# Optimization experiments

Measured on AMD Instinct MI355X. Metric: run time of the kernel, lower is better.

The kernel has to match this reference:

```python
import jax, jax.numpy as jnp
import numpy as np

B, L, H, KV, D, HID = 2, 2048, 16, 4, 128, 2048
EPS = 1e-6
ROPE_BASE = 10000.0


def _rotate_half(x):
    x1, x2 = jnp.split(x, 2, axis=-1)
    return jnp.concatenate((-x2, x1), axis=-1)


def _rms_norm(x, w):
    xf = x.astype(jnp.float32)
    var = jnp.mean(xf * xf, axis=-1, keepdims=True)
    return w * (xf * jax.lax.rsqrt(var + EPS)).astype(x.dtype)


def setup_inputs() -> dict:
    key = jax.random.key(0)
    ks = jax.random.split(key, 6)
    hidden_states = jax.random.normal(ks[0], (B, L, HID), dtype=jnp.float32)
    # rotary embeddings (standard rope table)
    inv_freq = 1.0 / (ROPE_BASE ** (jnp.arange(0, D, 2, dtype=jnp.float32) / D))
    pos = jnp.arange(L, dtype=jnp.float32)
    freqs = pos[:, None] * inv_freq[None, :]          # [L, D/2]
    emb = jnp.concatenate((freqs, freqs), axis=-1)    # [L, D]
    cos = jnp.broadcast_to(jnp.cos(emb)[None], (B, L, D))
    sin = jnp.broadcast_to(jnp.sin(emb)[None], (B, L, D))
    s = 0.02
    Wq = jax.random.normal(ks[1], (HID, H * D), dtype=jnp.float32) * s
    Wk = jax.random.normal(ks[2], (HID, KV * D), dtype=jnp.float32) * s
    Wv = jax.random.normal(ks[3], (HID, KV * D), dtype=jnp.float32) * s
    Wo = jax.random.normal(ks[4], (H * D, HID), dtype=jnp.float32) * s
    q_norm_w = jnp.ones((D,), dtype=jnp.float32)
    k_norm_w = jnp.ones((D,), dtype=jnp.float32)
    return {"hidden_states": hidden_states, "cos": cos, "sin": sin,
            "Wq": Wq, "Wk": Wk, "Wv": Wv, "Wo": Wo,
            "q_norm_w": q_norm_w, "k_norm_w": k_norm_w}


def reference(hidden_states, cos, sin, Wq, Wk, Wv, Wo, q_norm_w, k_norm_w):
    scale = D ** -0.5
    n_rep = H // KV
    q = (hidden_states @ Wq).reshape(B, L, H, D)
    k = (hidden_states @ Wk).reshape(B, L, KV, D)
    v = (hidden_states @ Wv).reshape(B, L, KV, D)
    q = _rms_norm(q, q_norm_w).transpose(0, 2, 1, 3)   # [B,H,L,D]
    k = _rms_norm(k, k_norm_w).transpose(0, 2, 1, 3)   # [B,KV,L,D]
    v = v.transpose(0, 2, 1, 3)                         # [B,KV,L,D]
    c = cos[:, None]                                    # [B,1,L,D]
    s = sin[:, None]
    q = q * c + _rotate_half(q) * s
    k = k * c + _rotate_half(k) * s
    # GQA without materializing repeated K/V: group query heads per kv head.
    qg = q.reshape(B, KV, n_rep, L, D)
    scores = jnp.einsum('bgrld,bgmd->bgrlm', qg, k) * scale
    attn = jax.nn.softmax(scores, axis=-1)
    out = jnp.einsum('bgrlm,bgmd->bgrld', attn, v)      # [B,KV,n_rep,L,D]
    out = out.reshape(B, H, L, D).transpose(0, 2, 1, 3).reshape(B, L, H * D)
    return out @ Wo
```

## Files before the change

kernel.cpp:

```cpp
#include <hip/hip_runtime.h>

typedef unsigned short u16;
typedef unsigned int u32;
typedef short bf16x8 __attribute__((ext_vector_type(8)));
typedef float f32x4 __attribute__((ext_vector_type(4)));

#define B_ 2
#define L_ 2048
#define H_ 16
#define KV_ 4
#define D_ 128
#define HID_ 2048

#define QSCALE (0.08838834764831845f * 1.4426950408889634f)
#define SMAX 17.0f

__device__ __forceinline__ u16 f2bf(float f) {
  union { float f; u32 u; } v; v.f = f;
  u32 u = v.u;
  return (u16)((u + 0x7FFFu + ((u >> 16) & 1u)) >> 16);
}
__device__ __forceinline__ float bf2f(u16 h) {
  union { u32 u; float f; } v; v.u = ((u32)h) << 16;
  return v.f;
}
__device__ __forceinline__ u32 pkbf(float a, float b) {
  union { float f; u32 u; } x, y; x.f = a; y.f = b;
  return ((x.u + 0x8000u) >> 16) | ((y.u + 0x8000u) & 0xffff0000u);
}
__device__ __forceinline__ void gl_lds16(const void* g, void* l) {
  __builtin_amdgcn_global_load_lds((__attribute__((address_space(1))) void*)(g),
                                   (__attribute__((address_space(3))) void*)(l),
                                   16, 0, 0);
}

__global__ void k_f2b(const float* __restrict__ src, u16* __restrict__ dst, int n4) {
  int i = blockIdx.x * 256 + threadIdx.x;
  if (i >= n4) return;
  float4 v = ((const float4*)src)[i];
  u32 a = (u32)f2bf(v.x) | ((u32)f2bf(v.y) << 16);
  u32 b = (u32)f2bf(v.z) | ((u32)f2bf(v.w) << 16);
  ((uint2*)dst)[i] = make_uint2(a, b);
}

__global__ void k_tconv_all(const float* __restrict__ Wq, const float* __restrict__ Wk,
                            const float* __restrict__ Wv, const float* __restrict__ Wo,
                            u16* __restrict__ Wtqkv, u16* __restrict__ Wto) {
  __shared__ float t[32][33];
  int id = blockIdx.x;
  const float* src; u16* dst; int C; int ct, rt;
  if (id < 4096)      { src = Wq; dst = Wtqkv;               C = 2048; ct = id & 63; rt = id >> 6; }
  else if (id < 5120) { id -= 4096; src = Wk; dst = Wtqkv + 2048 * 2048; C = 512; ct = id & 15; rt = id >> 4; }
  else if (id < 6144) { id -= 5120; src = Wv; dst = Wtqkv + 2560 * 2048; C = 512; ct = id & 15; rt = id >> 4; }
  else                { id -= 6144; src = Wo; dst = Wto;     C = 2048; ct = id & 63; rt = id >> 6; }
  const int R = 2048;
  int c0 = ct * 32, r0 = rt * 32;
  for (int i = threadIdx.y; i < 32; i += 8)
    t[i][threadIdx.x] = src[(size_t)(r0 + i) * C + c0 + threadIdx.x];
  __syncthreads();
  for (int i = threadIdx.y; i < 32; i += 8)
    dst[(size_t)(c0 + i) * R + r0 + threadIdx.x] = f2bf(t[threadIdx.x][i]);
}

template <int OUT_BF16>
__global__ __launch_bounds__(256, 3) void k_gemm_bt(
    const u16* __restrict__ A, const u16* __restrict__ Bt, void* __restrict__ Cv,
    int M, int N, int K) {
  __shared__ u16 smem[16384];
  u16* As = smem;
  u16* Bs = smem + 8192;
  const int tid = threadIdx.x;
  const int wave = tid >> 6, lane = tid & 63;
  const int wr = wave >> 1, wc = wave & 1;
  const int quad = lane >> 4, fm = lane & 15;
  const int m0 = blockIdx.y * 128, n0 = blockIdx.x * 128;
  f32x4 acc[4][4];
  for (int i = 0; i < 4; ++i)
    for (int j = 0; j < 4; ++j)
      for (int r = 0; r < 4; ++r) acc[i][j][r] = 0.0f;

  const int lrow = lane >> 3;
  const int lcol = (lane & 7) * 8;
  const int fk = quad * 8;

  for (int kt = 0; kt < K; kt += 64) {
    for (int p = 0; p < 4; ++p) {
      int roff = wave * 32 + p * 8 + lrow;
      gl_lds16(A + (size_t)(m0 + roff) * K + kt + lcol,
               As + wave * 2048 + p * 512 + lane * 8);
      gl_lds16(Bt + (size_t)(n0 + roff) * K + kt + lcol,
               Bs + wave * 2048 + p * 512 + lane * 8);
    }
    __syncthreads();
    for (int s = 0; s < 2; ++s) {
      bf16x8 af[4], bfr[4];
      for (int i = 0; i < 4; ++i)
        af[i] = *(const bf16x8*)(As + (wr * 64 + i * 16 + fm) * 64 + s * 32 + fk);
      for (int j = 0; j < 4; ++j)
        bfr[j] = *(const bf16x8*)(Bs + (wc * 64 + j * 16 + fm) * 64 + s * 32 + fk);
      for (int i = 0; i < 4; ++i)
        for (int j = 0; j < 4; ++j)
          acc[i][j] = __builtin_amdgcn_mfma_f32_16x16x32_bf16(af[i], bfr[j],
                                                              acc[i][j], 0, 0, 0);
    }
    __syncthreads();
  }

  if (OUT_BF16) {
    u16* Cs = smem;
    for (int hh = 0; hh < 2; ++hh) {
      if (hh) __syncthreads();
      if (wr == hh)
        for (int i = 0; i < 4; ++i)
          for (int j = 0; j < 4; ++j)
            for (int r = 0; r < 4; ++r)
              Cs[(i * 16 + quad * 4 + r) * 136 + wc * 64 + j * 16 + fm] =
                  f2bf(acc[i][j][r]);
      __syncthreads();
      for (int it = 0; it < 4; ++it) {
        int row = it * 16 + (tid >> 4);
        int col = (tid & 15) * 8;
        uint4 v = *(const uint4*)(Cs + row * 136 + col);
        *(uint4*)((u16*)Cv + (size_t)(m0 + hh * 64 + row) * N + n0 + col) = v;
      }
    }
  } else {
    float* Cf = (float*)smem;
    for (int p = 0; p < 4; ++p) {
      if (p) __syncthreads();
      if (wr == (p >> 1))
        for (int ii = 0; ii < 2; ++ii) {
          int i = 2 * (p & 1) + ii;
          for (int j = 0; j < 4; ++j)
            for (int r = 0; r < 4; ++r)
              Cf[(ii * 16 + quad * 4 + r) * 132 + wc * 64 + j * 16 + fm] =
                  acc[i][j][r];
        }
      __syncthreads();
      for (int it = 0; it < 4; ++it) {
        int row = it * 8 + (tid >> 5);
        int col = (tid & 31) * 4;
        float4 v = *(const float4*)(Cf + row * 132 + col);
        *(float4*)((float*)Cv + (size_t)(m0 + p * 32 + row) * N + n0 + col) = v;
      }
    }
  }
}

__global__ __launch_bounds__(256) void k_norm_rope(
    const u16* __restrict__ qkv, const float* __restrict__ cosp,
    const float* __restrict__ sinp, const float* __restrict__ qw,
    const float* __restrict__ kw, u16* __restrict__ Qb, u16* __restrict__ Kb,
    u16* __restrict__ Vtb) {
  int wid = blockIdx.x * 4 + (threadIdx.x >> 6);
  int lane = threadIdx.x & 63;
  int tok = wid / 24, unit = wid % 24;
  int b = tok >> 11, l = tok & 2047;
  const u16* row = qkv + (size_t)tok * 3072;
  int d0 = lane * 2;
  if (unit < 20) {
    int isq = unit < 16;
    int col = isq ? unit * 128 : 2048 + (unit - 16) * 128;
    u32 u = *(const u32*)(row + col + d0);
    float x0 = bf2f((u16)(u & 0xffff)), x1 = bf2f((u16)(u >> 16));
    float ss = x0 * x0 + x1 * x1;
    for (int m = 1; m < 64; m <<= 1) ss += __shfl_xor(ss, m);
    float rr = rsqrtf(ss * (1.0f / 128.0f) + 1e-6f);
    const float* wv = isq ? qw : kw;
    float n0 = x0 * rr * wv[d0], n1 = x1 * rr * wv[d0 + 1];
    float p0 = __shfl_xor(n0, 32), p1 = __shfl_xor(n1, 32);
    float sgn = (lane < 32) ? -1.0f : 1.0f;
    const float* cb = cosp + (size_t)tok * 128;
    const float* sb = sinp + (size_t)tok * 128;
    float o0 = n0 * cb[d0] + sgn * p0 * sb[d0];
    float o1 = n1 * cb[d0 + 1] + sgn * p1 * sb[d0 + 1];
    if (isq) {
      o0 *= QSCALE;
      o1 *= QSCALE;
      u32 packed = (u32)f2bf(o0) | ((u32)f2bf(o1) << 16);
      size_t off = (((size_t)(b * H_ + unit)) * L_ + l) * D_ + d0;
      *(u32*)(Qb + off) = packed;
    } else {
      u32 packed = (u32)f2bf(o0) | ((u32)f2bf(o1) << 16);
      size_t off = (((size_t)(b * KV_ + (unit - 16))) * L_ + l) * D_ + d0;
      *(u32*)(Kb + off) = packed;
    }
  } else {
    int g = unit - 20;
    int lp = (l & ~31) | (((l >> 2) & 3) << 3) | (((l >> 4) & 1) << 2) | (l & 3);
    size_t base = (((size_t)(b * KV_ + g)) * D_ + d0) * L_ + lp;
    Vtb[base] = row[2560 + g * 128 + d0];
    Vtb[base + L_] = row[2560 + g * 128 + d0 + 1];
  }
}

__global__ __launch_bounds__(256, 2) void k_attn(const u16* __restrict__ Qb,
                                                 const u16* __restrict__ Kb,
                                                 const u16* __restrict__ Vtb,
                                                 u16* __restrict__ AO) {
  __shared__ u16 smem[16384];
  u16* Ks = smem;
  u16* Vs = smem + 8192;
  const int tid = threadIdx.x, wave = tid >> 6, lane = tid & 63;
  const int quad = lane >> 4, fm = lane & 15;
  const int f7 = fm & 7;
  const int qt = blockIdx.x, bh = blockIdx.y;
  const int b = bh >> 4, h = bh & 15, g = h >> 2;
  const u16* Kg = Kb + ((size_t)(b * KV_ + g)) * L_ * D_;
  const u16* Vg = Vtb + ((size_t)(b * KV_ + g)) * D_ * L_;

  const u16* Qg = Qb + ((size_t)bh * L_ + qt * 128 + wave * 32 + fm) * D_;
  bf16x8 qf1[4], qf2[4];
  for (int ks = 0; ks < 4; ++ks) {
    qf1[ks] = *(const bf16x8*)(Qg + ks * 32 + quad * 8);
    qf2[ks] = *(const bf16x8*)(Qg + 16 * D_ + ks * 32 + quad * 8);
  }

  f32x4 o1[8], o2[8];
  for (int f = 0; f < 8; ++f)
    for (int r = 0; r < 4; ++r) { o1[f][r] = 0.0f; o2[f][r] = 0.0f; }
  float lr1 = 0.0f, lr2 = 0.0f;

  const int eK = wave * 2048 + (lane << 3);
  const int cK = lane & 15;
  const int cV = lane & 7;
  for (int kt = 0; kt < 32; ++kt) {
    __syncthreads();
    for (int p = 0; p < 4; ++p) {
      int e = eK + p * 512;
      int rowK = e >> 7;
      int gK = (cK & 8) | ((cK & 7) ^ (rowK & 7));
      gl_lds16(Kg + (size_t)(kt * 64 + rowK) * 128 + gK * 8, Ks + e);
      int rowV = e >> 6;
      int gV = cV ^ (rowV & 7);
      gl_lds16(Vg + (size_t)rowV * L_ + kt * 64 + gV * 8, Vs + e);
    }
    __syncthreads();

    f32x4 s1[4], s2[4];
    for (int n = 0; n < 4; ++n)
      for (int r = 0; r < 4; ++r) { s1[n][r] = 0.0f; s2[n][r] = 0.0f; }
    for (int ks = 0; ks < 4; ++ks) {
      int c = 4 * ks + quad;
      int cp = (c & 8) | ((c & 7) ^ f7);
      for (int n = 0; n < 4; ++n) {
        bf16x8 kf = *(const bf16x8*)(Ks + (n * 16 + fm) * 128 + cp * 8);
        s1[n] = __builtin_amdgcn_mfma_f32_16x16x32_bf16(kf, qf1[ks], s1[n], 0, 0, 0);
        s2[n] = __builtin_amdgcn_mfma_f32_16x16x32_bf16(kf, qf2[ks], s2[n], 0, 0, 0);
      }
    }

    u32 pk1[4][2], pk2[4][2];
    float rs1 = 0.0f, rs2 = 0.0f;
    for (int n = 0; n < 4; ++n) {
      float a0 = __builtin_amdgcn_exp2f(s1[n][0] - SMAX);
      float a1 = __builtin_amdgcn_exp2f(s1[n][1] - SMAX);
      float a2 = __builtin_amdgcn_exp2f(s1[n][2] - SMAX);
      float a3 = __builtin_amdgcn_exp2f(s1[n][3] - SMAX);
      rs1 += (a0 + a1) + (a2 + a3);
      pk1[n][0] = pkbf(a0, a1);
      pk1[n][1] = pkbf(a2, a3);
      float b0 = __builtin_amdgcn_exp2f(s2[n][0] - SMAX);
      float b1 = __builtin_amdgcn_exp2f(s2[n][1] - SMAX);
      float b2 = __builtin_amdgcn_exp2f(s2[n][2] - SMAX);
      float b3 = __builtin_amdgcn_exp2f(s2[n][3] - SMAX);
      rs2 += (b0 + b1) + (b2 + b3);
      pk2[n][0] = pkbf(b0, b1);
      pk2[n][1] = pkbf(b2, b3);
    }
    lr1 += rs1;
    lr2 += rs2;

    for (int ks2 = 0; ks2 < 2; ++ks2) {
      union { u32 u[4]; bf16x8 v; } pa1, pa2;
      pa1.u[0] = pk1[2 * ks2][0];
      pa1.u[1] = pk1[2 * ks2][1];
      pa1.u[2] = pk1[2 * ks2 + 1][0];
      pa1.u[3] = pk1[2 * ks2 + 1][1];
      pa2.u[0] = pk2[2 * ks2][0];
      pa2.u[1] = pk2[2 * ks2][1];
      pa2.u[2] = pk2[2 * ks2 + 1][0];
      pa2.u[3] = pk2[2 * ks2 + 1][1];
      int chunk = (4 * ks2 + quad) ^ f7;
      for (int f = 0; f < 8; ++f) {
        bf16x8 vv = *(const bf16x8*)(Vs + (f * 16 + fm) * 64 + chunk * 8);
        o1[f] = __builtin_amdgcn_mfma_f32_16x16x32_bf16(pa1.v, vv, o1[f], 0, 0, 0);
        o2[f] = __builtin_amdgcn_mfma_f32_16x16x32_bf16(pa2.v, vv, o2[f], 0, 0, 0);
      }
    }
  }

  const size_t tok0 = (size_t)b * L_ + qt * 128;
  for (int grp = 0; grp < 2; ++grp) {
    f32x4* o = grp ? o2 : o1;
    float lr = grp ? lr2 : lr1;
    lr += __shfl_xor(lr, 16);
    lr += __shfl_xor(lr, 32);
    float li = 1.0f / lr;
    float l0 = __shfl(li, (lane & 48) | (quad * 4 + 0));
    float l1 = __shfl(li, (lane & 48) | (quad * 4 + 1));
    float l2 = __shfl(li, (lane & 48) | (quad * 4 + 2));
    float l3 = __shfl(li, (lane & 48) | (quad * 4 + 3));
    __syncthreads();
    for (int f = 0; f < 8; ++f) {
      int e = (wave * 16 + quad * 4) * 136 + f * 16 + fm;
      smem[e] = f2bf(o[f][0] * l0);
      smem[e + 136] = f2bf(o[f][1] * l1);
      smem[e + 272] = f2bf(o[f][2] * l2);
      smem[e + 408] = f2bf(o[f][3] * l3);
    }
    __syncthreads();
    for (int it = 0; it < 8; ++it) {
      int crow = (tid >> 6) * 16 + it * 2 + (lane >> 5);
      int q = (crow >> 4) * 32 + grp * 16 + (crow & 15);
      int cc = (lane & 31) * 4;
      uint2 v = *(const uint2*)(smem + crow * 136 + cc);
      *(uint2*)(AO + (tok0 + q) * (H_ * D_) + h * D_ + cc) = v;
    }
  }
}

extern "C" void kernel_launch(void* const* d_in, const int* in_sizes, int n_in,
                              void* d_out, int out_size, void* d_ws,
                              size_t ws_size, hipStream_t stream) {
  const float* hidden = (const float*)d_in[0];
  const float* cosp = (const float*)d_in[1];
  const float* sinp = (const float*)d_in[2];
  const float* Wq = (const float*)d_in[3];
  const float* Wk = (const float*)d_in[4];
  const float* Wv = (const float*)d_in[5];
  const float* Wo = (const float*)d_in[6];
  const float* qw = (const float*)d_in[7];
  const float* kw = (const float*)d_in[8];
  float* out = (float*)d_out;

  char* w = (char*)d_ws;
  u16* Xb = (u16*)(w);
  u16* Wtqkv = (u16*)(w + (16u << 20));
  u16* Wto = (u16*)(w + (28u << 20));
  u16* qkv = (u16*)(w + (36u << 20));
  u16* Qb = (u16*)(w + (60u << 20));
  u16* Kb = (u16*)(w + (76u << 20));
  u16* Vtb = (u16*)(w + (80u << 20));
  u16* AO = Xb;

  k_f2b<<<8192, 256, 0, stream>>>(hidden, Xb, 2097152);
  k_tconv_all<<<10240, dim3(32, 8), 0, stream>>>(Wq, Wk, Wv, Wo, Wtqkv, Wto);
  k_gemm_bt<1><<<dim3(24, 32), 256, 0, stream>>>(Xb, Wtqkv, qkv, 4096, 3072, 2048);
  k_norm_rope<<<24576, 256, 0, stream>>>(qkv, cosp, sinp, qw, kw, Qb, Kb, Vtb);
  k_attn<<<dim3(16, 32), 256, 0, stream>>>(Qb, Kb, Vtb, AO);
  k_gemm_bt<0><<<dim3(16, 32), 256, 0, stream>>>(AO, Wto, out, 4096, 2048, 2048);
}
```

Measured before the change: 339.8 us.

## Double-buffer attention K/V tiles, split V transpose, merge prep kernels

The attention kernel now holds two LDS buffers and issues the asynchronous global-to-LDS loads for the next K/V tile before computing on the current one. This removes one barrier per iteration and lets memory traffic overlap MFMA work, at the cost of doubling LDS use per block. The V transpose moves out of the norm/rope kernel into a dedicated kernel that stages tiles through LDS, so the strided scalar stores become wider contiguous ones. The hidden-state conversion and weight transpose kernels are merged into one launch. The overlap may be lost if the compiler waits on all outstanding LDS-DMA loads before each LDS read.

Result: no change. 337.0 us (-0.8%).

```diff
diff --git a/kernel.cpp b/kernel.cpp
--- a/kernel.cpp
+++ b/kernel.cpp
@@ -34,20 +34,21 @@
                                    16, 0, 0);
 }
 
-__global__ void k_f2b(const float* __restrict__ src, u16* __restrict__ dst, int n4) {
-  int i = blockIdx.x * 256 + threadIdx.x;
-  if (i >= n4) return;
-  float4 v = ((const float4*)src)[i];
-  u32 a = (u32)f2bf(v.x) | ((u32)f2bf(v.y) << 16);
-  u32 b = (u32)f2bf(v.z) | ((u32)f2bf(v.w) << 16);
-  ((uint2*)dst)[i] = make_uint2(a, b);
-}
-
-__global__ void k_tconv_all(const float* __restrict__ Wq, const float* __restrict__ Wk,
-                            const float* __restrict__ Wv, const float* __restrict__ Wo,
-                            u16* __restrict__ Wtqkv, u16* __restrict__ Wto) {
+__global__ void k_prep(const float* __restrict__ hidden, u16* __restrict__ Xb,
+                       const float* __restrict__ Wq, const float* __restrict__ Wk,
+                       const float* __restrict__ Wv, const float* __restrict__ Wo,
+                       u16* __restrict__ Wtqkv, u16* __restrict__ Wto) {
   __shared__ float t[32][33];
   int id = blockIdx.x;
+  if (id < 8192) {
+    int i = id * 256 + threadIdx.x;
+    float4 v = ((const float4*)hidden)[i];
+    u32 a = (u32)f2bf(v.x) | ((u32)f2bf(v.y) << 16);
+    u32 b = (u32)f2bf(v.z) | ((u32)f2bf(v.w) << 16);
+    ((uint2*)Xb)[i] = make_uint2(a, b);
+    return;
+  }
+  id -= 8192;
   const float* src; u16* dst; int C; int ct, rt;
   if (id < 4096)      { src = Wq; dst = Wtqkv;               C = 2048; ct = id & 63; rt = id >> 6; }
   else if (id < 5120) { id -= 4096; src = Wk; dst = Wtqkv + 2048 * 2048; C = 512; ct = id & 15; rt = id >> 4; }
@@ -55,11 +56,12 @@
   else                { id -= 6144; src = Wo; dst = Wto;     C = 2048; ct = id & 63; rt = id >> 6; }
   const int R = 2048;
   int c0 = ct * 32, r0 = rt * 32;
-  for (int i = threadIdx.y; i < 32; i += 8)
-    t[i][threadIdx.x] = src[(size_t)(r0 + i) * C + c0 + threadIdx.x];
+  int tx = threadIdx.x & 31, ty = threadIdx.x >> 5;
+  for (int i = ty; i < 32; i += 8)
+    t[i][tx] = src[(size_t)(r0 + i) * C + c0 + tx];
   __syncthreads();
-  for (int i = threadIdx.y; i < 32; i += 8)
-    dst[(size_t)(c0 + i) * R + r0 + threadIdx.x] = f2bf(t[threadIdx.x][i]);
+  for (int i = ty; i < 32; i += 8)
+    dst[(size_t)(c0 + i) * R + r0 + tx] = f2bf(t[tx][i]);
 }
 
 template <int OUT_BF16>
@@ -150,47 +152,63 @@
 __global__ __launch_bounds__(256) void k_norm_rope(
     const u16* __restrict__ qkv, const float* __restrict__ cosp,
     const float* __restrict__ sinp, const float* __restrict__ qw,
-    const float* __restrict__ kw, u16* __restrict__ Qb, u16* __restrict__ Kb,
-    u16* __restrict__ Vtb) {
+    const float* __restrict__ kw, u16* __restrict__ Qb, u16* __restrict__ Kb) {
   int wid = blockIdx.x * 4 + (threadIdx.x >> 6);
   int lane = threadIdx.x & 63;
-  int tok = wid / 24, unit = wid % 24;
+  int tok = wid / 20, unit = wid % 20;
   int b = tok >> 11, l = tok & 2047;
   const u16* row = qkv + (size_t)tok * 3072;
   int d0 = lane * 2;
-  if (unit < 20) {
-    int isq = unit < 16;
-    int col = isq ? unit * 128 : 2048 + (unit - 16) * 128;
-    u32 u = *(const u32*)(row + col + d0);
-    float x0 = bf2f((u16)(u & 0xffff)), x1 = bf2f((u16)(u >> 16));
-    float ss = x0 * x0 + x1 * x1;
-    for (int m = 1; m < 64; m <<= 1) ss += __shfl_xor(ss, m);
-    float rr = rsqrtf(ss * (1.0f / 128.0f) + 1e-6f);
-    const float* wv = isq ? qw : kw;
-    float n0 = x0 * rr * wv[d0], n1 = x1 * rr * wv[d0 + 1];
-    float p0 = __shfl_xor(n0, 32), p1 = __shfl_xor(n1, 32);
-    float sgn = (lane < 32) ? -1.0f : 1.0f;
-    const float* cb = cosp + (size_t)tok * 128;
-    const float* sb = sinp + (size_t)tok * 128;
-    float o0 = n0 * cb[d0] + sgn * p0 * sb[d0];
-    float o1 = n1 * cb[d0 + 1] + sgn * p1 * sb[d0 + 1];
-    if (isq) {
-      o0 *= QSCALE;
-      o1 *= QSCALE;
-      u32 packed = (u32)f2bf(o0) | ((u32)f2bf(o1) << 16);
-      size_t off = (((size_t)(b * H_ + unit)) * L_ + l) * D_ + d0;
-      *(u32*)(Qb + off) = packed;
-    } else {
-      u32 packed = (u32)f2bf(o0) | ((u32)f2bf(o1) << 16);
-      size_t off = (((size_t)(b * KV_ + (unit - 16))) * L_ + l) * D_ + d0;
-      *(u32*)(Kb + off) = packed;
-    }
+  int isq = unit < 16;
+  int col = isq ? unit * 128 : 2048 + (unit - 16) * 128;
+  u32 u = *(const u32*)(row + col + d0);
+  float x0 = bf2f((u16)(u & 0xffff)), x1 = bf2f((u16)(u >> 16));
+  float ss = x0 * x0 + x1 * x1;
+  for (int m = 1; m < 64; m <<= 1) ss += __shfl_xor(ss, m);
+  float rr = rsqrtf(ss * (1.0f / 128.0f) + 1e-6f);
+  const float* wv = isq ? qw : kw;
+  float n0 = x0 * rr * wv[d0], n1 = x1 * rr * wv[d0 + 1];
+  float p0 = __shfl_xor(n0, 32), p1 = __shfl_xor(n1, 32);
+  float sgn = (lane < 32) ? -1.0f : 1.0f;
+  const float* cb = cosp + (size_t)tok * 128;
+  const float* sb = sinp + (size_t)tok * 128;
+  float o0 = n0 * cb[d0] + sgn * p0 * sb[d0];
+  float o1 = n1 * cb[d0 + 1] + sgn * p1 * sb[d0 + 1];
+  if (isq) {
+    o0 *= QSCALE;
+    o1 *= QSCALE;
+    u32 packed = (u32)f2bf(o0) | ((u32)f2bf(o1) << 16);
+    size_t off = (((size_t)(b * H_ + unit)) * L_ + l) * D_ + d0;
+    *(u32*)(Qb + off) = packed;
   } else {
-    int g = unit - 20;
-    int lp = (l & ~31) | (((l >> 2) & 3) << 3) | (((l >> 4) & 1) << 2) | (l & 3);
-    size_t base = (((size_t)(b * KV_ + g)) * D_ + d0) * L_ + lp;
-    Vtb[base] = row[2560 + g * 128 + d0];
-    Vtb[base + L_] = row[2560 + g * 128 + d0 + 1];
+    u32 packed = (u32)f2bf(o0) | ((u32)f2bf(o1) << 16);
+    size_t off = (((size_t)(b * KV_ + (unit - 16))) * L_ + l) * D_ + d0;
+    *(u32*)(Kb + off) = packed;
+  }
+}
+
+__global__ __launch_bounds__(256) void k_vtrans(const u16* __restrict__ qkv,
+                                                u16* __restrict__ Vtb) {
+  __shared__ u16 t[64][136];
+  int blk = blockIdx.x;
+  int lt = blk & 31, g = (blk >> 5) & 3, b = blk >> 7;
+  int l0 = lt * 64;
+  for (int p = 0; p < 4; ++p) {
+    int idx = p * 256 + threadIdx.x;
+    int r = idx >> 4, co = (idx & 15) * 8;
+    uint4 v = *(const uint4*)(qkv + (size_t)(b * 2048 + l0 + r) * 3072 + 2560 +
+                              g * 128 + co);
+    *(uint4*)(&t[r][co]) = v;
+  }
+  __syncthreads();
+  int d = threadIdx.x >> 1, lh = threadIdx.x & 1;
+  u16* dst = Vtb + (((size_t)(b * KV_ + g)) * D_ + d) * L_ + l0 + lh * 32;
+  for (int bc = 0; bc < 8; ++bc) {
+    int bb = bc & 1, c = bc >> 1;
+    int ls = lh * 32 + 16 * bb + 4 * c;
+    u32 lo = (u32)t[ls][d] | ((u32)t[ls + 1][d] << 16);
+    u32 hi = (u32)t[ls + 2][d] | ((u32)t[ls + 3][d] << 16);
+    *(uint2*)(dst + 8 * c + 4 * bb) = make_uint2(lo, hi);
   }
 }
 
@@ -198,9 +216,7 @@
                                                  const u16* __restrict__ Kb,
                                                  const u16* __restrict__ Vtb,
                                                  u16* __restrict__ AO) {
-  __shared__ u16 smem[16384];
-  u16* Ks = smem;
-  u16* Vs = smem + 8192;
+  __shared__ u16 smem[32768];
   const int tid = threadIdx.x, wave = tid >> 6, lane = tid & 63;
   const int quad = lane >> 4, fm = lane & 15;
   const int f7 = fm & 7;
@@ -224,18 +240,28 @@
   const int eK = wave * 2048 + (lane << 3);
   const int cK = lane & 15;
   const int cV = lane & 7;
+
+#define STAGE(kt_, buf_)                                                      \
+  {                                                                           \
+    u16* Kd = smem + (buf_)*16384;                                            \
+    u16* Vd = smem + (buf_)*16384 + 8192;                                     \
+    for (int p = 0; p < 4; ++p) {                                             \
+      int e = eK + p * 512;                                                   \
+      int rowK = e >> 7;                                                      \
+      int gK = (cK & 8) | ((cK & 7) ^ (rowK & 7));                            \
+      gl_lds16(Kg + (size_t)((kt_)*64 + rowK) * 128 + gK * 8, Kd + e);        \
+      int rowV = e >> 6;                                                      \
+      int gV = cV ^ (rowV & 7);                                               \
+      gl_lds16(Vg + (size_t)rowV * L_ + (kt_)*64 + gV * 8, Vd + e);           \
+    }                                                                         \
+  }
+
+  STAGE(0, 0);
   for (int kt = 0; kt < 32; ++kt) {
     __syncthreads();
-    for (int p = 0; p < 4; ++p) {
-      int e = eK + p * 512;
-      int rowK = e >> 7;
-      int gK = (cK & 8) | ((cK & 7) ^ (rowK & 7));
-      gl_lds16(Kg + (size_t)(kt * 64 + rowK) * 128 + gK * 8, Ks + e);
-      int rowV = e >> 6;
-      int gV = cV ^ (rowV & 7);
-      gl_lds16(Vg + (size_t)rowV * L_ + kt * 64 + gV * 8, Vs + e);
-    }
-    __syncthreads();
+    if (kt + 1 < 32) STAGE(kt + 1, (kt + 1) & 1);
+    const u16* Ks = smem + (kt & 1) * 16384;
+    const u16* Vs = Ks + 8192;
 
     f32x4 s1[4], s2[4];
     for (int n = 0; n < 4; ++n)
@@ -289,6 +315,7 @@
       }
     }
   }
+#undef STAGE
 
   const size_t tok0 = (size_t)b * L_ + qt * 128;
   for (int grp = 0; grp < 2; ++grp) {
@@ -344,10 +371,10 @@
   u16* Vtb = (u16*)(w + (80u << 20));
   u16* AO = Xb;
 
-  k_f2b<<<8192, 256, 0, stream>>>(hidden, Xb, 2097152);
-  k_tconv_all<<<10240, dim3(32, 8), 0, stream>>>(Wq, Wk, Wv, Wo, Wtqkv, Wto);
+  k_prep<<<18432, 256, 0, stream>>>(hidden, Xb, Wq, Wk, Wv, Wo, Wtqkv, Wto);
   k_gemm_bt<1><<<dim3(24, 32), 256, 0, stream>>>(Xb, Wtqkv, qkv, 4096, 3072, 2048);
-  k_norm_rope<<<24576, 256, 0, stream>>>(qkv, cosp, sinp, qw, kw, Qb, Kb, Vtb);
+  k_norm_rope<<<20480, 256, 0, stream>>>(qkv, cosp, sinp, qw, kw, Qb, Kb);
+  k_vtrans<<<256, 256, 0, stream>>>(qkv, Vtb);
   k_attn<<<dim3(16, 32), 256, 0, stream>>>(Qb, Kb, Vtb, AO);
   k_gemm_bt<0><<<dim3(16, 32), 256, 0, stream>>>(AO, Wto, out, 4096, 2048, 2048);
 }
```
